# Optimization experiments

Hardware: AMD Instinct MI355X
Metric: run time of the kernel (lower is better)

## Reference

```python
import jax, jax.numpy as jnp
import numpy as np

BINS = 10
MIU = 0.02
SHAPE = (8, 160, 160, 36)  # (batch, h, w, num_anchors*4)


def setup_inputs() -> dict:
    key = jax.random.key(0)
    k1, k2, k3 = jax.random.split(key, 3)
    delta_targets = jax.random.normal(k1, SHAPE, dtype=jnp.float32)
    deltas = jax.random.normal(k2, SHAPE, dtype=jnp.float32)
    delta_weights = (jax.random.uniform(k3, SHAPE) < 0.3).astype(jnp.float32)
    return {"delta_targets": delta_targets, "deltas": deltas, "delta_weights": delta_weights}


def reference(delta_targets, deltas, delta_weights):
    # bin edges: [0, 0.1, ..., 0.9, 1.0 + 1e-6]
    edges = jnp.arange(BINS + 1, dtype=jnp.float32) / BINS
    edges = edges.at[BINS].add(1e-6)

    diff = deltas - delta_targets
    denom = jnp.sqrt(diff * diff + MIU * MIU)
    asl1 = denom - MIU                       # authentic smooth L1 (ASL1)
    grads = jnp.abs(diff / denom)            # gradient norm, in [0, 1)

    total_num = jnp.maximum(jnp.sum(delta_weights), 1.0)
    valid = delta_weights > 0

    # per-element bin index: edges[i] <= g < edges[i+1]
    idx = jnp.clip(jnp.digitize(grads.ravel(), edges) - 1, 0, BINS - 1)
    # histogram of valid elements per bin (replaces the 10 masked reduce_sums)
    counts = jax.ops.segment_sum(valid.ravel().astype(jnp.float32), idx, num_segments=BINS)

    n_nonempty = jnp.sum(counts > 0).astype(jnp.float32)
    per_bin_w = jnp.where(counts > 0, total_num / jnp.maximum(counts, 1.0), 0.0)

    beta = jnp.where(valid, per_bin_w[idx].reshape(grads.shape), 0.0)
    beta = beta / jnp.maximum(n_nonempty, 1.0)

    return asl1 * beta / total_num
```

## Files before the change

### kernel.cpp

```cpp
#include <hip/hip_runtime.h>

#define NBINS 10
#define PROW 16
#define MAXBLOCKS 4096

#define PARAMS_OFF (MAXBLOCKS * PROW)

__device__ __forceinline__ int bin_of(float g) {
    int b = 0;
    b += g >= 0.1f; b += g >= 0.2f; b += g >= 0.3f;
    b += g >= 0.4f; b += g >= 0.5f; b += g >= 0.6f;
    b += g >= 0.7f; b += g >= 0.8f; b += g >= 0.9f;
    return b;
}

__device__ __forceinline__ void hist_elem(float a, float b, float w,
                                          float& wsum, int* cnt) {
    float d = b - a;
    float denom = sqrtf(d * d + 0.0004f);
    float g = fabsf(d / denom);
    wsum += w;
    bool valid = w > 0.0f;
    int bin = bin_of(g);
#pragma unroll
    for (int k = 0; k < NBINS; ++k)
        cnt[k] += (valid && bin == k) ? 1 : 0;
}

__global__ __launch_bounds__(256) void ghmr_hist(
    const float* __restrict__ dt, const float* __restrict__ dl,
    const float* __restrict__ dw, int n, float* __restrict__ partials)
{
    const int tid = blockIdx.x * blockDim.x + threadIdx.x;
    const int nthreads = gridDim.x * blockDim.x;
    const int n4 = n >> 2;

    const float4* dt4 = (const float4*)dt;
    const float4* dl4 = (const float4*)dl;
    const float4* dw4 = (const float4*)dw;

    float wsum = 0.0f;
    int cnt[NBINS];
#pragma unroll
    for (int k = 0; k < NBINS; ++k) cnt[k] = 0;

    for (int i = tid; i < n4; i += nthreads) {
        float4 a = dt4[i];
        float4 b = dl4[i];
        float4 w = dw4[i];
        hist_elem(a.x, b.x, w.x, wsum, cnt);
        hist_elem(a.y, b.y, w.y, wsum, cnt);
        hist_elem(a.z, b.z, w.z, wsum, cnt);
        hist_elem(a.w, b.w, w.w, wsum, cnt);
    }
    for (int i = (n4 << 2) + tid; i < n; i += nthreads)
        hist_elem(dt[i], dl[i], dw[i], wsum, cnt);

#pragma unroll
    for (int off = 32; off > 0; off >>= 1) {
        wsum += __shfl_down(wsum, off);
#pragma unroll
        for (int k = 0; k < NBINS; ++k) cnt[k] += __shfl_down(cnt[k], off);
    }

    __shared__ float s_w[4];
    __shared__ int   s_c[4][NBINS];
    const int lane = threadIdx.x & 63;
    const int wave = threadIdx.x >> 6;
    if (lane == 0) {
        s_w[wave] = wsum;
#pragma unroll
        for (int k = 0; k < NBINS; ++k) s_c[wave][k] = cnt[k];
    }
    __syncthreads();
    if (threadIdx.x == 0)
        partials[blockIdx.x * PROW] = s_w[0] + s_w[1] + s_w[2] + s_w[3];
    if (threadIdx.x < NBINS) {
        int tc = s_c[0][threadIdx.x] + s_c[1][threadIdx.x] +
                 s_c[2][threadIdx.x] + s_c[3][threadIdx.x];
        partials[blockIdx.x * PROW + 1 + threadIdx.x] = (float)tc;
    }
}

__global__ __launch_bounds__(256) void ghmr_finalize(
    const float* __restrict__ partials, int nblocks, float* __restrict__ params)
{
    float acc[NBINS + 1];
#pragma unroll
    for (int k = 0; k <= NBINS; ++k) acc[k] = 0.0f;
    for (int r = threadIdx.x; r < nblocks; r += 256) {
        const float* row = partials + r * PROW;
#pragma unroll
        for (int k = 0; k <= NBINS; ++k) acc[k] += row[k];
    }
#pragma unroll
    for (int off = 32; off > 0; off >>= 1)
#pragma unroll
        for (int k = 0; k <= NBINS; ++k) acc[k] += __shfl_down(acc[k], off);

    __shared__ float s_acc[4][NBINS + 1];
    const int lane = threadIdx.x & 63;
    const int wave = threadIdx.x >> 6;
    if (lane == 0)
#pragma unroll
        for (int k = 0; k <= NBINS; ++k) s_acc[wave][k] = acc[k];
    __syncthreads();

    if (threadIdx.x == 0) {
        float total = fmaxf(s_acc[0][0] + s_acc[1][0] + s_acc[2][0] + s_acc[3][0], 1.0f);
        float cf[NBINS];
        int nne = 0;
#pragma unroll
        for (int b = 0; b < NBINS; ++b) {
            cf[b] = s_acc[0][b + 1] + s_acc[1][b + 1] + s_acc[2][b + 1] + s_acc[3][b + 1];
            nne += (cf[b] > 0.0f) ? 1 : 0;
        }
        float nnef = fmaxf((float)nne, 1.0f);
#pragma unroll
        for (int b = 0; b < NBINS; ++b) {
            float pbw = (cf[b] > 0.0f) ? (total / fmaxf(cf[b], 1.0f)) : 0.0f;
            params[b] = pbw / nnef / total;
        }
    }
}

__device__ __forceinline__ float apply_elem(float a, float b, float w,
                                            const float* sb) {
    float d = b - a;
    float denom = sqrtf(d * d + 0.0004f);
    float g = fabsf(d / denom);
    float asl1 = denom - 0.02f;
    float r = 0.0f;
    if (w > 0.0f) r = asl1 * sb[bin_of(g)];
    return r;
}

__global__ __launch_bounds__(256) void ghmr_apply(
    const float* __restrict__ dt, const float* __restrict__ dl,
    const float* __restrict__ dw, const float* __restrict__ params,
    float* __restrict__ out, int n)
{
    __shared__ float sb[NBINS];
    if (threadIdx.x < NBINS) sb[threadIdx.x] = params[threadIdx.x];
    __syncthreads();

    const int tid = blockIdx.x * blockDim.x + threadIdx.x;
    const int nthreads = gridDim.x * blockDim.x;
    const int n4 = n >> 2;

    const float4* dt4 = (const float4*)dt;
    const float4* dl4 = (const float4*)dl;
    const float4* dw4 = (const float4*)dw;
    float4* out4 = (float4*)out;

    for (int i = tid; i < n4; i += nthreads) {
        float4 a = dt4[i];
        float4 b = dl4[i];
        float4 w = dw4[i];
        float4 r;
        r.x = apply_elem(a.x, b.x, w.x, sb);
        r.y = apply_elem(a.y, b.y, w.y, sb);
        r.z = apply_elem(a.z, b.z, w.z, sb);
        r.w = apply_elem(a.w, b.w, w.w, sb);
        out4[i] = r;
    }
    for (int i = (n4 << 2) + tid; i < n; i += nthreads)
        out[i] = apply_elem(dt[i], dl[i], dw[i], sb);
}

extern "C" void kernel_launch(void* const* d_in, const int* in_sizes, int n_in,
                              void* d_out, int out_size, void* d_ws, size_t ws_size,
                              hipStream_t stream) {
    const float* dt = (const float*)d_in[0];
    const float* dl = (const float*)d_in[1];
    const float* dw = (const float*)d_in[2];
    float* out = (float*)d_out;
    const int n = in_sizes[0];

    float* ws_f = (float*)d_ws;
    float* partials = ws_f;
    float* params = ws_f + PARAMS_OFF;

    int n4 = n >> 2;
    int blocks = (n4 + 255) / 256;
    if (blocks > 2048) blocks = 2048;
    if (blocks < 1) blocks = 1;

    ghmr_hist<<<blocks, 256, 0, stream>>>(dt, dl, dw, n, partials);
    ghmr_finalize<<<1, 256, 0, stream>>>(partials, blocks, params);
    ghmr_apply<<<blocks, 256, 0, stream>>>(dt, dl, dw, params, out, n);
}
```

Baseline: 145.2 us.

## Fuse histogram, finalize and apply into one cooperative kernel with register-cached values

Replaces the three-kernel pipeline with a single cooperative kernel that computes the histogram, grid-syncs, derives per-bin weights in each block, and writes outputs. Each thread keeps up to 8 float4 iterations of ASL1 values and packed bin indices in registers, so the apply phase does not re-read the three input arrays. This removes about half the global memory traffic and two kernel launches. In exchange it adds a grid-wide barrier and higher register pressure, with a fallback to the old three-kernel path if the cooperative launch fails.

```diff
diff --git a/kernel.cpp b/kernel.cpp
--- a/kernel.cpp
+++ b/kernel.cpp
@@ -1,10 +1,15 @@
 #include <hip/hip_runtime.h>
+#include <hip/hip_cooperative_groups.h>
+
+namespace cg = cooperative_groups;
 
 #define NBINS 10
+#define TPB 256
+#define MAX_BLOCKS 1024
+#define FB_BLOCKS 2048
+#define MAX_ITERS 8
 #define PROW 16
-#define MAXBLOCKS 4096
-
-#define PARAMS_OFF (MAXBLOCKS * PROW)
+#define PARAMS_OFF (4096 * PROW)
 
 __device__ __forceinline__ int bin_of(float g) {
     int b = 0;
@@ -12,6 +17,23 @@
     b += g >= 0.4f; b += g >= 0.5f; b += g >= 0.6f;
     b += g >= 0.7f; b += g >= 0.8f; b += g >= 0.9f;
     return b;
+}
+
+__device__ __forceinline__ float p1_elem(float a, float b, float w,
+                                         float& wsum, int* cnt,
+                                         unsigned int& pk, int shift) {
+    float d = b - a;
+    float denom = sqrtf(d * d + 0.0004f);
+    float g = fabsf(d / denom);
+    wsum += w;
+    bool valid = w > 0.0f;
+    int bin = bin_of(g);
+    int idx = valid ? bin : NBINS;
+    pk |= (unsigned int)idx << shift;
+#pragma unroll
+    for (int k = 0; k < NBINS; ++k)
+        cnt[k] += (valid && bin == k) ? 1 : 0;
+    return denom - 0.02f;
 }
 
 __device__ __forceinline__ void hist_elem(float a, float b, float w,
@@ -27,6 +49,159 @@
         cnt[k] += (valid && bin == k) ? 1 : 0;
 }
 
+__global__ __launch_bounds__(TPB, 4) void ghmr_fused(
+    const float* __restrict__ dt, const float* __restrict__ dl,
+    const float* __restrict__ dw, float* __restrict__ partials,
+    float* __restrict__ out, int n)
+{
+    const int nblocks = gridDim.x;
+    const int nthreads = nblocks * TPB;
+    const int tid = blockIdx.x * TPB + threadIdx.x;
+    const int n4 = n >> 2;
+
+    const float4* dt4 = (const float4*)dt;
+    const float4* dl4 = (const float4*)dl;
+    const float4* dw4 = (const float4*)dw;
+    float4* out4 = (float4*)out;
+
+    float wsum = 0.0f;
+    int cnt[NBINS];
+#pragma unroll
+    for (int k = 0; k < NBINS; ++k) cnt[k] = 0;
+
+    float asl1v[MAX_ITERS][4];
+    unsigned int pk[MAX_ITERS];
+#pragma unroll
+    for (int it = 0; it < MAX_ITERS; ++it) pk[it] = 0;
+
+#pragma unroll
+    for (int it = 0; it < MAX_ITERS; ++it) {
+        int q = tid + it * nthreads;
+        if (q < n4) {
+            float4 a = dt4[q];
+            float4 b = dl4[q];
+            float4 w = dw4[q];
+            asl1v[it][0] = p1_elem(a.x, b.x, w.x, wsum, cnt, pk[it], 0);
+            asl1v[it][1] = p1_elem(a.y, b.y, w.y, wsum, cnt, pk[it], 4);
+            asl1v[it][2] = p1_elem(a.z, b.z, w.z, wsum, cnt, pk[it], 8);
+            asl1v[it][3] = p1_elem(a.w, b.w, w.w, wsum, cnt, pk[it], 12);
+        }
+    }
+    for (int q = tid + MAX_ITERS * nthreads; q < n4; q += nthreads) {
+        float4 a = dt4[q]; float4 b = dl4[q]; float4 w = dw4[q];
+        hist_elem(a.x, b.x, w.x, wsum, cnt);
+        hist_elem(a.y, b.y, w.y, wsum, cnt);
+        hist_elem(a.z, b.z, w.z, wsum, cnt);
+        hist_elem(a.w, b.w, w.w, wsum, cnt);
+    }
+    for (int i = (n4 << 2) + tid; i < n; i += nthreads)
+        hist_elem(dt[i], dl[i], dw[i], wsum, cnt);
+
+#pragma unroll
+    for (int off = 32; off > 0; off >>= 1) {
+        wsum += __shfl_down(wsum, off);
+#pragma unroll
+        for (int k = 0; k < NBINS; ++k) cnt[k] += __shfl_down(cnt[k], off);
+    }
+    __shared__ float s_w[4];
+    __shared__ int   s_c[4][NBINS];
+    {
+        const int lane = threadIdx.x & 63;
+        const int wave = threadIdx.x >> 6;
+        if (lane == 0) {
+            s_w[wave] = wsum;
+#pragma unroll
+            for (int k = 0; k < NBINS; ++k) s_c[wave][k] = cnt[k];
+        }
+    }
+    __syncthreads();
+    if (threadIdx.x == 0)
+        partials[blockIdx.x * PROW] = s_w[0] + s_w[1] + s_w[2] + s_w[3];
+    if (threadIdx.x < NBINS) {
+        int tc = s_c[0][threadIdx.x] + s_c[1][threadIdx.x] +
+                 s_c[2][threadIdx.x] + s_c[3][threadIdx.x];
+        partials[blockIdx.x * PROW + 1 + threadIdx.x] = (float)tc;
+    }
+
+    __threadfence();
+    cg::this_grid().sync();
+
+    float acc[NBINS + 1];
+#pragma unroll
+    for (int k = 0; k <= NBINS; ++k) acc[k] = 0.0f;
+    for (int r = threadIdx.x; r < nblocks; r += TPB) {
+        const float* row = partials + r * PROW;
+#pragma unroll
+        for (int k = 0; k <= NBINS; ++k) acc[k] += row[k];
+    }
+#pragma unroll
+    for (int off = 32; off > 0; off >>= 1)
+#pragma unroll
+        for (int k = 0; k <= NBINS; ++k) acc[k] += __shfl_down(acc[k], off);
+
+    __shared__ float s_acc[4][NBINS + 1];
+    __shared__ float s_sb[NBINS + 1];
+    {
+        const int lane = threadIdx.x & 63;
+        const int wave = threadIdx.x >> 6;
+        if (lane == 0)
+#pragma unroll
+            for (int k = 0; k <= NBINS; ++k) s_acc[wave][k] = acc[k];
+    }
+    __syncthreads();
+    if (threadIdx.x == 0) {
+        float total = fmaxf(s_acc[0][0] + s_acc[1][0] + s_acc[2][0] + s_acc[3][0], 1.0f);
+        float cf[NBINS];
+        int nne = 0;
+#pragma unroll
+        for (int b = 0; b < NBINS; ++b) {
+            cf[b] = s_acc[0][b + 1] + s_acc[1][b + 1] + s_acc[2][b + 1] + s_acc[3][b + 1];
+            nne += (cf[b] > 0.0f) ? 1 : 0;
+        }
+        float nnef = fmaxf((float)nne, 1.0f);
+#pragma unroll
+        for (int b = 0; b < NBINS; ++b) {
+            float pbw = (cf[b] > 0.0f) ? (total / fmaxf(cf[b], 1.0f)) : 0.0f;
+            s_sb[b] = pbw / nnef / total;
+        }
+        s_sb[NBINS] = 0.0f;
+    }
+    __syncthreads();
+
+#pragma unroll
+    for (int it = 0; it < MAX_ITERS; ++it) {
+        int q = tid + it * nthreads;
+        if (q < n4) {
+            unsigned int p = pk[it];
+            float4 r;
+            r.x = asl1v[it][0] * s_sb[p & 0xF];
+            r.y = asl1v[it][1] * s_sb[(p >> 4) & 0xF];
+            r.z = asl1v[it][2] * s_sb[(p >> 8) & 0xF];
+            r.w = asl1v[it][3] * s_sb[(p >> 12) & 0xF];
+            out4[q] = r;
+        }
+    }
+    for (int q = tid + MAX_ITERS * nthreads; q < n4; q += nthreads) {
+        float4 a = dt4[q]; float4 b = dl4[q]; float4 w = dw4[q];
+        float4 r;
+        { float d = b.x-a.x; float dn = sqrtf(d*d+0.0004f); float g = fabsf(d/dn);
+          r.x = (w.x > 0.0f) ? (dn - 0.02f) * s_sb[bin_of(g)] : 0.0f; }
+        { float d = b.y-a.y; float dn = sqrtf(d*d+0.0004f); float g = fabsf(d/dn);
+          r.y = (w.y > 0.0f) ? (dn - 0.02f) * s_sb[bin_of(g)] : 0.0f; }
+        { float d = b.z-a.z; float dn = sqrtf(d*d+0.0004f); float g = fabsf(d/dn);
+          r.z = (w.z > 0.0f) ? (dn - 0.02f) * s_sb[bin_of(g)] : 0.0f; }
+        { float d = b.w-a.w; float dn = sqrtf(d*d+0.0004f); float g = fabsf(d/dn);
+          r.w = (w.w > 0.0f) ? (dn - 0.02f) * s_sb[bin_of(g)] : 0.0f; }
+        out4[q] = r;
+    }
+    for (int i = (n4 << 2) + tid; i < n; i += nthreads) {
+        float d = dl[i] - dt[i];
+        float dn = sqrtf(d*d + 0.0004f);
+        float g = fabsf(d/dn);
+        out[i] = (dw[i] > 0.0f) ? (dn - 0.02f) * s_sb[bin_of(g)] : 0.0f;
+    }
+}
+
 __global__ __launch_bounds__(256) void ghmr_hist(
     const float* __restrict__ dt, const float* __restrict__ dl,
     const float* __restrict__ dw, int n, float* __restrict__ partials)
@@ -34,7 +209,6 @@
     const int tid = blockIdx.x * blockDim.x + threadIdx.x;
     const int nthreads = gridDim.x * blockDim.x;
     const int n4 = n >> 2;
-
     const float4* dt4 = (const float4*)dt;
     const float4* dl4 = (const float4*)dl;
     const float4* dw4 = (const float4*)dw;
@@ -45,9 +219,7 @@
     for (int k = 0; k < NBINS; ++k) cnt[k] = 0;
 
     for (int i = tid; i < n4; i += nthreads) {
-        float4 a = dt4[i];
-        float4 b = dl4[i];
-        float4 w = dw4[i];
+        float4 a = dt4[i]; float4 b = dl4[i]; float4 w = dw4[i];
         hist_elem(a.x, b.x, w.x, wsum, cnt);
         hist_elem(a.y, b.y, w.y, wsum, cnt);
         hist_elem(a.z, b.z, w.z, wsum, cnt);
@@ -62,7 +234,6 @@
 #pragma unroll
         for (int k = 0; k < NBINS; ++k) cnt[k] += __shfl_down(cnt[k], off);
     }
-
     __shared__ float s_w[4];
     __shared__ int   s_c[4][NBINS];
     const int lane = threadIdx.x & 63;
@@ -121,18 +292,8 @@
             float pbw = (cf[b] > 0.0f) ? (total / fmaxf(cf[b], 1.0f)) : 0.0f;
             params[b] = pbw / nnef / total;
         }
-    }
-}
-
-__device__ __forceinline__ float apply_elem(float a, float b, float w,
-                                            const float* sb) {
-    float d = b - a;
-    float denom = sqrtf(d * d + 0.0004f);
-    float g = fabsf(d / denom);
-    float asl1 = denom - 0.02f;
-    float r = 0.0f;
-    if (w > 0.0f) r = asl1 * sb[bin_of(g)];
-    return r;
+        params[NBINS] = 0.0f;
+    }
 }
 
 __global__ __launch_bounds__(256) void ghmr_apply(
@@ -140,32 +301,37 @@
     const float* __restrict__ dw, const float* __restrict__ params,
     float* __restrict__ out, int n)
 {
-    __shared__ float sb[NBINS];
-    if (threadIdx.x < NBINS) sb[threadIdx.x] = params[threadIdx.x];
+    __shared__ float sb[NBINS + 1];
+    if (threadIdx.x <= NBINS) sb[threadIdx.x] = params[threadIdx.x];
     __syncthreads();
 
     const int tid = blockIdx.x * blockDim.x + threadIdx.x;
     const int nthreads = gridDim.x * blockDim.x;
     const int n4 = n >> 2;
-
     const float4* dt4 = (const float4*)dt;
     const float4* dl4 = (const float4*)dl;
     const float4* dw4 = (const float4*)dw;
     float4* out4 = (float4*)out;
 
     for (int i = tid; i < n4; i += nthreads) {
-        float4 a = dt4[i];
-        float4 b = dl4[i];
-        float4 w = dw4[i];
+        float4 a = dt4[i]; float4 b = dl4[i]; float4 w = dw4[i];
         float4 r;
-        r.x = apply_elem(a.x, b.x, w.x, sb);
-        r.y = apply_elem(a.y, b.y, w.y, sb);
-        r.z = apply_elem(a.z, b.z, w.z, sb);
-        r.w = apply_elem(a.w, b.w, w.w, sb);
+        { float d = b.x-a.x; float dn = sqrtf(d*d+0.0004f); float g = fabsf(d/dn);
+          r.x = (w.x > 0.0f) ? (dn - 0.02f) * sb[bin_of(g)] : 0.0f; }
+        { float d = b.y-a.y; float dn = sqrtf(d*d+0.0004f); float g = fabsf(d/dn);
+          r.y = (w.y > 0.0f) ? (dn - 0.02f) * sb[bin_of(g)] : 0.0f; }
+        { float d = b.z-a.z; float dn = sqrtf(d*d+0.0004f); float g = fabsf(d/dn);
+          r.z = (w.z > 0.0f) ? (dn - 0.02f) * sb[bin_of(g)] : 0.0f; }
+        { float d = b.w-a.w; float dn = sqrtf(d*d+0.0004f); float g = fabsf(d/dn);
+          r.w = (w.w > 0.0f) ? (dn - 0.02f) * sb[bin_of(g)] : 0.0f; }
         out4[i] = r;
     }
-    for (int i = (n4 << 2) + tid; i < n; i += nthreads)
-        out[i] = apply_elem(dt[i], dl[i], dw[i], sb);
+    for (int i = (n4 << 2) + tid; i < n; i += nthreads) {
+        float d = dl[i] - dt[i];
+        float dn = sqrtf(d*d + 0.0004f);
+        float g = fabsf(d/dn);
+        out[i] = (dw[i] > 0.0f) ? (dn - 0.02f) * sb[bin_of(g)] : 0.0f;
+    }
 }
 
 extern "C" void kernel_launch(void* const* d_in, const int* in_sizes, int n_in,
@@ -175,18 +341,28 @@
     const float* dl = (const float*)d_in[1];
     const float* dw = (const float*)d_in[2];
     float* out = (float*)d_out;
-    const int n = in_sizes[0];
-
-    float* ws_f = (float*)d_ws;
-    float* partials = ws_f;
-    float* params = ws_f + PARAMS_OFF;
-
-    int n4 = n >> 2;
-    int blocks = (n4 + 255) / 256;
-    if (blocks > 2048) blocks = 2048;
+    float* partials = (float*)d_ws;
+    float* params = (float*)d_ws + PARAMS_OFF;
+    int n = in_sizes[0];
+
+    int occ = 0;
+    hipError_t oe = hipOccupancyMaxActiveBlocksPerMultiprocessor(
+        &occ, ghmr_fused, TPB, 0);
+    int blocks = MAX_BLOCKS;
+    if (oe == hipSuccess && occ > 0) {
+        int cap = occ * 256;
+        if (cap < blocks) blocks = cap;
+    }
     if (blocks < 1) blocks = 1;
 
-    ghmr_hist<<<blocks, 256, 0, stream>>>(dt, dl, dw, n, partials);
-    ghmr_finalize<<<1, 256, 0, stream>>>(partials, blocks, params);
-    ghmr_apply<<<blocks, 256, 0, stream>>>(dt, dl, dw, params, out, n);
-}
+    void* args[] = { (void*)&dt, (void*)&dl, (void*)&dw,
+                     (void*)&partials, (void*)&out, (void*)&n };
+    hipError_t le = hipLaunchCooperativeKernel((const void*)ghmr_fused,
+                                               dim3(blocks), dim3(TPB),
+                                               args, 0, stream);
+    if (le != hipSuccess) {
+        ghmr_hist<<<FB_BLOCKS, 256, 0, stream>>>(dt, dl, dw, n, partials);
+        ghmr_finalize<<<1, 256, 0, stream>>>(partials, FB_BLOCKS, params);
+        ghmr_apply<<<FB_BLOCKS, 256, 0, stream>>>(dt, dl, dw, params, out, n);
+    }
+}
```

Result: slower. 228.1 us (+57.1%).

## Pack ASL1 loss and bin index in pass one, apply in a fused second pass

Applied to the files above, without the earlier changes.

The first pass now computes the ASL1 loss and gradient bin for each element and writes both into one 32-bit word: the low 4 mantissa bits carry the bin index, or an invalid marker. The second pass reads only that packed array instead of re-reading all three inputs and recomputing sqrt and divide. The separate finalize kernel is folded into the second pass, with every block redundantly reducing the 1024 partial rows. Per-thread histogram counts are packed into 6-bit fields of a u64, and the grid is fixed at 1024 blocks; this drops a little precision from the loss and would overflow silently if one thread handled more than 63 valid elements per bin.

```diff
diff --git a/kernel.cpp b/kernel.cpp
--- a/kernel.cpp
+++ b/kernel.cpp
@@ -1,60 +1,56 @@
 #include <hip/hip_runtime.h>
 
 #define NBINS 10
+#define TPB 256
+#define PBLOCKS 1024
 #define PROW 16
-#define MAXBLOCKS 4096
+#define PACKED_OFF (1 << 18)
 
-#define PARAMS_OFF (MAXBLOCKS * PROW)
+typedef unsigned long long u64;
 
-__device__ __forceinline__ int bin_of(float g) {
-    int b = 0;
-    b += g >= 0.1f; b += g >= 0.2f; b += g >= 0.3f;
-    b += g >= 0.4f; b += g >= 0.5f; b += g >= 0.6f;
-    b += g >= 0.7f; b += g >= 0.8f; b += g >= 0.9f;
-    return b;
+__device__ __forceinline__ unsigned int pack_elem(float a, float b, float w,
+                                                  float& wsum, u64& h) {
+    float d = b - a;
+    float dn = sqrtf(d * d + 0.0004f);
+    float g = fabsf(d / dn);
+    wsum += w;
+    bool valid = w > 0.0f;
+    int bin = 0;
+    bin += g >= 0.1f; bin += g >= 0.2f; bin += g >= 0.3f;
+    bin += g >= 0.4f; bin += g >= 0.5f; bin += g >= 0.6f;
+    bin += g >= 0.7f; bin += g >= 0.8f; bin += g >= 0.9f;
+    h += (u64)valid << (bin * 6);
+    int idx = valid ? bin : NBINS;
+    float asl1 = dn - 0.02f;
+    return (__float_as_uint(asl1) & 0xFFFFFFF0u) | (unsigned int)idx;
 }
 
-__device__ __forceinline__ void hist_elem(float a, float b, float w,
-                                          float& wsum, int* cnt) {
-    float d = b - a;
-    float denom = sqrtf(d * d + 0.0004f);
-    float g = fabsf(d / denom);
-    wsum += w;
-    bool valid = w > 0.0f;
-    int bin = bin_of(g);
-#pragma unroll
-    for (int k = 0; k < NBINS; ++k)
-        cnt[k] += (valid && bin == k) ? 1 : 0;
-}
-
-__global__ __launch_bounds__(256) void ghmr_hist(
-    const float* __restrict__ dt, const float* __restrict__ dl,
-    const float* __restrict__ dw, int n, float* __restrict__ partials)
+__global__ __launch_bounds__(TPB) void ghmr_pass1(
+    const float4* __restrict__ dt4, const float4* __restrict__ dl4,
+    const float4* __restrict__ dw4, uint4* __restrict__ packed,
+    float* __restrict__ partials, int n4)
 {
-    const int tid = blockIdx.x * blockDim.x + threadIdx.x;
-    const int nthreads = gridDim.x * blockDim.x;
-    const int n4 = n >> 2;
-
-    const float4* dt4 = (const float4*)dt;
-    const float4* dl4 = (const float4*)dl;
-    const float4* dw4 = (const float4*)dw;
+    const int tid = blockIdx.x * TPB + threadIdx.x;
+    const int stride = PBLOCKS * TPB;
 
     float wsum = 0.0f;
+    u64 h = 0ULL;
+
+    for (int q = tid; q < n4; q += stride) {
+        float4 a = dt4[q];
+        float4 b = dl4[q];
+        float4 w = dw4[q];
+        uint4 p;
+        p.x = pack_elem(a.x, b.x, w.x, wsum, h);
+        p.y = pack_elem(a.y, b.y, w.y, wsum, h);
+        p.z = pack_elem(a.z, b.z, w.z, wsum, h);
+        p.w = pack_elem(a.w, b.w, w.w, wsum, h);
+        packed[q] = p;
+    }
+
     int cnt[NBINS];
 #pragma unroll
-    for (int k = 0; k < NBINS; ++k) cnt[k] = 0;
-
-    for (int i = tid; i < n4; i += nthreads) {
-        float4 a = dt4[i];
-        float4 b = dl4[i];
-        float4 w = dw4[i];
-        hist_elem(a.x, b.x, w.x, wsum, cnt);
-        hist_elem(a.y, b.y, w.y, wsum, cnt);
-        hist_elem(a.z, b.z, w.z, wsum, cnt);
-        hist_elem(a.w, b.w, w.w, wsum, cnt);
-    }
-    for (int i = (n4 << 2) + tid; i < n; i += nthreads)
-        hist_elem(dt[i], dl[i], dw[i], wsum, cnt);
+    for (int k = 0; k < NBINS; ++k) cnt[k] = (int)((h >> (6 * k)) & 63ULL);
 
 #pragma unroll
     for (int off = 32; off > 0; off >>= 1) {
@@ -82,13 +78,14 @@
     }
 }
 
-__global__ __launch_bounds__(256) void ghmr_finalize(
-    const float* __restrict__ partials, int nblocks, float* __restrict__ params)
+__global__ __launch_bounds__(TPB) void ghmr_pass2(
+    const uint4* __restrict__ packed, const float* __restrict__ partials,
+    float4* __restrict__ out4, int n4)
 {
     float acc[NBINS + 1];
 #pragma unroll
     for (int k = 0; k <= NBINS; ++k) acc[k] = 0.0f;
-    for (int r = threadIdx.x; r < nblocks; r += 256) {
+    for (int r = threadIdx.x; r < PBLOCKS; r += TPB) {
         const float* row = partials + r * PROW;
 #pragma unroll
         for (int k = 0; k <= NBINS; ++k) acc[k] += row[k];
@@ -99,6 +96,7 @@
         for (int k = 0; k <= NBINS; ++k) acc[k] += __shfl_down(acc[k], off);
 
     __shared__ float s_acc[4][NBINS + 1];
+    __shared__ float s_sb[NBINS + 1];
     const int lane = threadIdx.x & 63;
     const int wave = threadIdx.x >> 6;
     if (lane == 0)
@@ -119,53 +117,49 @@
 #pragma unroll
         for (int b = 0; b < NBINS; ++b) {
             float pbw = (cf[b] > 0.0f) ? (total / fmaxf(cf[b], 1.0f)) : 0.0f;
-            params[b] = pbw / nnef / total;
+            s_sb[b] = pbw / nnef / total;
         }
+        s_sb[NBINS] = 0.0f;
+    }
+    __syncthreads();
+
+    const int tid = blockIdx.x * TPB + threadIdx.x;
+    const int stride = PBLOCKS * TPB;
+    for (int q = tid; q < n4; q += stride) {
+        uint4 p = packed[q];
+        float4 r;
+        r.x = __uint_as_float(p.x & 0xFFFFFFF0u) * s_sb[p.x & 0xFu];
+        r.y = __uint_as_float(p.y & 0xFFFFFFF0u) * s_sb[p.y & 0xFu];
+        r.z = __uint_as_float(p.z & 0xFFFFFFF0u) * s_sb[p.z & 0xFu];
+        r.w = __uint_as_float(p.w & 0xFFFFFFF0u) * s_sb[p.w & 0xFu];
+        out4[q] = r;
     }
 }
 
-__device__ __forceinline__ float apply_elem(float a, float b, float w,
-                                            const float* sb) {
-    float d = b - a;
-    float denom = sqrtf(d * d + 0.0004f);
-    float g = fabsf(d / denom);
-    float asl1 = denom - 0.02f;
-    float r = 0.0f;
-    if (w > 0.0f) r = asl1 * sb[bin_of(g)];
-    return r;
-}
-
-__global__ __launch_bounds__(256) void ghmr_apply(
-    const float* __restrict__ dt, const float* __restrict__ dl,
-    const float* __restrict__ dw, const float* __restrict__ params,
-    float* __restrict__ out, int n)
+__global__ void ghmr_tail(const float* __restrict__ dt, const float* __restrict__ dl,
+                          const float* __restrict__ dw, const float* __restrict__ partials,
+                          float* __restrict__ out, int n, int n4)
 {
-    __shared__ float sb[NBINS];
-    if (threadIdx.x < NBINS) sb[threadIdx.x] = params[threadIdx.x];
-    __syncthreads();
-
-    const int tid = blockIdx.x * blockDim.x + threadIdx.x;
-    const int nthreads = gridDim.x * blockDim.x;
-    const int n4 = n >> 2;
-
-    const float4* dt4 = (const float4*)dt;
-    const float4* dl4 = (const float4*)dl;
-    const float4* dw4 = (const float4*)dw;
-    float4* out4 = (float4*)out;
-
-    for (int i = tid; i < n4; i += nthreads) {
-        float4 a = dt4[i];
-        float4 b = dl4[i];
-        float4 w = dw4[i];
-        float4 r;
-        r.x = apply_elem(a.x, b.x, w.x, sb);
-        r.y = apply_elem(a.y, b.y, w.y, sb);
-        r.z = apply_elem(a.z, b.z, w.z, sb);
-        r.w = apply_elem(a.w, b.w, w.w, sb);
-        out4[i] = r;
+    float acc[NBINS + 1];
+    for (int k = 0; k <= NBINS; ++k) acc[k] = 0.0f;
+    for (int r = 0; r < PBLOCKS; ++r)
+        for (int k = 0; k <= NBINS; ++k) acc[k] += partials[r * PROW + k];
+    float total = fmaxf(acc[0], 1.0f);
+    int nne = 0;
+    for (int b = 0; b < NBINS; ++b) nne += (acc[b + 1] > 0.0f) ? 1 : 0;
+    float nnef = fmaxf((float)nne, 1.0f);
+    for (int i = (n4 << 2) + threadIdx.x; i < n; i += blockDim.x) {
+        float d = dl[i] - dt[i];
+        float dn = sqrtf(d * d + 0.0004f);
+        float g = fabsf(d / dn);
+        int bin = 0;
+        bin += g >= 0.1f; bin += g >= 0.2f; bin += g >= 0.3f;
+        bin += g >= 0.4f; bin += g >= 0.5f; bin += g >= 0.6f;
+        bin += g >= 0.7f; bin += g >= 0.8f; bin += g >= 0.9f;
+        float cf = acc[bin + 1];
+        float pbw = (cf > 0.0f) ? (total / fmaxf(cf, 1.0f)) : 0.0f;
+        out[i] = (dw[i] > 0.0f) ? (dn - 0.02f) * (pbw / nnef / total) : 0.0f;
     }
-    for (int i = (n4 << 2) + tid; i < n; i += nthreads)
-        out[i] = apply_elem(dt[i], dl[i], dw[i], sb);
 }
 
 extern "C" void kernel_launch(void* const* d_in, const int* in_sizes, int n_in,
@@ -175,18 +169,16 @@
     const float* dl = (const float*)d_in[1];
     const float* dw = (const float*)d_in[2];
     float* out = (float*)d_out;
+    float* partials = (float*)d_ws;
+    uint4* packed = (uint4*)((float*)d_ws + PACKED_OFF);
     const int n = in_sizes[0];
+    const int n4 = n >> 2;
 
-    float* ws_f = (float*)d_ws;
-    float* partials = ws_f;
-    float* params = ws_f + PARAMS_OFF;
-
-    int n4 = n >> 2;
-    int blocks = (n4 + 255) / 256;
-    if (blocks > 2048) blocks = 2048;
-    if (blocks < 1) blocks = 1;
-
-    ghmr_hist<<<blocks, 256, 0, stream>>>(dt, dl, dw, n, partials);
-    ghmr_finalize<<<1, 256, 0, stream>>>(partials, blocks, params);
-    ghmr_apply<<<blocks, 256, 0, stream>>>(dt, dl, dw, params, out, n);
+    ghmr_pass1<<<PBLOCKS, TPB, 0, stream>>>(
+        (const float4*)dt, (const float4*)dl, (const float4*)dw,
+        packed, partials, n4);
+    ghmr_pass2<<<PBLOCKS, TPB, 0, stream>>>(
+        packed, partials, (float4*)out, n4);
+    if (n & 3)
+        ghmr_tail<<<1, 256, 0, stream>>>(dt, dl, dw, partials, out, n, n4);
 }
```

New measurement: 133.6 us. 8.0% less time.
